# Performance work log

Measured on AMD Instinct MI355X. Metric: run time of the kernel, lower is better.

Reference implementation:

```python
import jax, jax.numpy as jnp
import numpy as np

T, B, F = 160, 640, 40
HID, PROJ, LAYERS = 768, 256, 3


def lstm_proj_layer(x, Wk, b, Wp, reverse=False):
    # x: [T, B, in]; Wk: [in+PROJ, 4*HID]; b: [4*HID]; Wp: [HID, PROJ]
    nb = x.shape[1]
    c0 = jnp.zeros((nb, HID), x.dtype)
    h0 = jnp.zeros((nb, PROJ), x.dtype)

    def step(carry, xt):
        c, h = carry
        z = jnp.concatenate([xt, h], axis=-1) @ Wk + b
        i, j, f, o = jnp.split(z, 4, axis=-1)  # TF LSTMCell gate order i,j,f,o
        c = jax.nn.sigmoid(f + 1.0) * c + jax.nn.sigmoid(i) * jnp.tanh(j)  # forget_bias=1.0
        h = (jax.nn.sigmoid(o) * jnp.tanh(c)) @ Wp  # projection
        return (c, h), h

    _, ys = jax.lax.scan(step, (c0, h0), x, reverse=reverse)
    return ys  # [T, B, PROJ], time-aligned with input even when reverse=True


def _run_stack(x, params, reverse):
    for (Wk, b, Wp) in params:
        x = lstm_proj_layer(x, Wk, b, Wp, reverse=reverse)
    return x


def setup_inputs() -> dict:
    key = jax.random.key(0)
    keys = jax.random.split(key, 1 + 6 * LAYERS)
    inp = {"batch": jax.random.normal(keys[0], (T, B, F), dtype=jnp.float32)}
    ki = 1
    for d in ("fw", "bw"):
        for l in range(LAYERS):
            in_dim = F if l == 0 else PROJ
            inp[f"Wk_{d}{l}"] = jax.random.normal(keys[ki], (in_dim + PROJ, 4 * HID), dtype=jnp.float32) * 0.05
            inp[f"b_{d}{l}"] = jnp.zeros((4 * HID,), dtype=jnp.float32)
            inp[f"Wp_{d}{l}"] = jax.random.normal(keys[ki + 1], (HID, PROJ), dtype=jnp.float32) * 0.05
            ki += 2
    return inp


def reference(batch,
              Wk_fw0, b_fw0, Wp_fw0, Wk_fw1, b_fw1, Wp_fw1, Wk_fw2, b_fw2, Wp_fw2,
              Wk_bw0, b_bw0, Wp_bw0, Wk_bw1, b_bw1, Wp_bw1, Wk_bw2, b_bw2, Wp_bw2):
    fw_params = [(Wk_fw0, b_fw0, Wp_fw0), (Wk_fw1, b_fw1, Wp_fw1), (Wk_fw2, b_fw2, Wp_fw2)]
    bw_params = [(Wk_bw0, b_bw0, Wp_bw0), (Wk_bw1, b_bw1, Wp_bw1), (Wk_bw2, b_bw2, Wp_bw2)]
    out_fw = _run_stack(batch, fw_params, reverse=False)
    out_bw = _run_stack(batch, bw_params, reverse=True)
    outputs = jnp.concatenate([out_fw, out_bw], axis=2)  # [T, B, 2*PROJ]
    embedded = (outputs[0] + outputs[-1]) / 2.0
    # tf.nn.l2_normalize semantics
    embedded = embedded * jax.lax.rsqrt(jnp.maximum(jnp.sum(embedded * embedded, axis=-1, keepdims=True), 1e-12))
    return embedded
```

## Files before the change

kernel.cpp:

```cpp
#include <hip/hip_runtime.h>


typedef _Float16 h8 __attribute__((ext_vector_type(8)));
typedef float f4 __attribute__((ext_vector_type(4)));

#define T_STEPS 160
#define NB 640
#define HID 768
#define PROJ 256
#define NGATE 3072

__device__ __forceinline__ float sigm(float x) { return 1.0f / (1.0f + __expf(-x)); }
__device__ __forceinline__ float tanh_fast(float x) { return 2.0f / (1.0f + __expf(-2.0f * x)) - 1.0f; }

struct GateArgs {
  const _Float16* A0[6];
  const _Float16* A1[6];
  const _Float16* Bw[6];
  const float*    bias[6];
  float*          cst[6];
  _Float16*       g[6];
  int w0[6];
  int lda0[6];
  int K[6];
  int act[6];
};

struct ProjArgs {
  const _Float16* G[6];
  const _Float16* Wp[6];
  _Float16* out[6];
  _Float16* out2[6];
  int act[6];
};

__global__ __launch_bounds__(512) void gate_step(GateArgs args) {
  const int z = blockIdx.z;
  if (!args.act[z]) return;

  __shared__ __align__(16) char sm[33280];
  _Float16 (*As)[72] = (_Float16(*)[72])sm;
  _Float16 (*Bs)[72] = (_Float16(*)[72])(sm + 18432);
  float (*zs)[65] = (float(*)[65])sm;

  const _Float16* A0 = args.A0[z];
  const _Float16* A1 = args.A1[z];
  const _Float16* Bw = args.Bw[z];
  const int w0 = args.w0[z], lda0 = args.lda0[z], K = args.K[z];
  const int n0 = blockIdx.x * 64;
  const int m0 = blockIdx.y * 128;
  const int tid = threadIdx.x;
  const int lane = tid & 63;
  const int wv = tid >> 6;
  const int wm = (wv & 3) * 32;
  const int wn = (wv >> 2) * 32;

  f4 acc[2][2] = {};

  const int lr = tid >> 3;
  const int lkg = (tid & 7) * 8;

  for (int k0 = 0; k0 < K; k0 += 64) {
    const int gk = k0 + lkg;
    h8 av0, av1;
    if (gk < w0) {
      av0 = *(const h8*)(A0 + (size_t)(m0 + lr) * lda0 + gk);
      av1 = *(const h8*)(A0 + (size_t)(m0 + lr + 64) * lda0 + gk);
    } else {
      av0 = *(const h8*)(A1 + (size_t)(m0 + lr) * 256 + (gk - w0));
      av1 = *(const h8*)(A1 + (size_t)(m0 + lr + 64) * 256 + (gk - w0));
    }
    h8 bv = *(const h8*)(Bw + (size_t)(n0 + lr) * K + gk);
    __syncthreads();
    *(h8*)&As[lr][lkg] = av0;
    *(h8*)&As[lr + 64][lkg] = av1;
    *(h8*)&Bs[lr][lkg] = bv;
    __syncthreads();
    const int mr = wm + (lane & 15);
    const int nr = wn + (lane & 15);
#pragma unroll
    for (int kk = 0; kk < 2; ++kk) {
      const int kq = ((lane >> 4) * 8) + kk * 32;
      h8 a0 = *(const h8*)&As[mr][kq];
      h8 a1 = *(const h8*)&As[mr + 16][kq];
      h8 b0 = *(const h8*)&Bs[nr][kq];
      h8 b1 = *(const h8*)&Bs[nr + 16][kq];
      acc[0][0] = __builtin_amdgcn_mfma_f32_16x16x32_f16(a0, b0, acc[0][0], 0, 0, 0);
      acc[0][1] = __builtin_amdgcn_mfma_f32_16x16x32_f16(a0, b1, acc[0][1], 0, 0, 0);
      acc[1][0] = __builtin_amdgcn_mfma_f32_16x16x32_f16(a1, b0, acc[1][0], 0, 0, 0);
      acc[1][1] = __builtin_amdgcn_mfma_f32_16x16x32_f16(a1, b1, acc[1][1], 0, 0, 0);
    }
  }

  __syncthreads();
#pragma unroll
  for (int mi = 0; mi < 2; ++mi)
#pragma unroll
    for (int ni = 0; ni < 2; ++ni)
#pragma unroll
      for (int r = 0; r < 4; ++r) {
        int row = wm + mi * 16 + ((lane >> 4) << 2) + r;
        int col = wn + ni * 16 + (lane & 15);
        zs[row][col] = acc[mi][ni][r];
      }
  __syncthreads();

  const float* bias = args.bias[z];
  float* cstate = args.cst[z];
  _Float16* gout = args.g[z];
  const int u0 = n0 >> 2;
#pragma unroll
  for (int it = 0; it < 4; ++it) {
    int item = it * 512 + tid;
    int row = item >> 4;
    int u = item & 15;
    float zi = zs[row][4 * u + 0] + bias[0 * HID + u0 + u];
    float zj = zs[row][4 * u + 1] + bias[1 * HID + u0 + u];
    float zf = zs[row][4 * u + 2] + bias[2 * HID + u0 + u];
    float zo = zs[row][4 * u + 3] + bias[3 * HID + u0 + u];
    size_t co = (size_t)(m0 + row) * HID + u0 + u;
    float cold = cstate[co];
    float cnew = sigm(zf + 1.0f) * cold + sigm(zi) * tanh_fast(zj);
    float g = sigm(zo) * tanh_fast(cnew);
    cstate[co] = cnew;
    gout[co] = (_Float16)g;
  }
}

__global__ __launch_bounds__(256) void proj_step(ProjArgs args) {
  const int z = blockIdx.z;
  if (!args.act[z]) return;

  __shared__ __align__(16) _Float16 As[64][72];
  __shared__ __align__(16) _Float16 Bs[64][72];

  const _Float16* A = args.G[z];
  const _Float16* B = args.Wp[z];
  const int n0 = blockIdx.x * 64;
  const int m0 = blockIdx.y * 64;
  const int tid = threadIdx.x;
  const int lane = tid & 63;
  const int wv = tid >> 6;
  const int wm = (wv & 1) * 32;
  const int wn = (wv >> 1) * 32;

  f4 acc[2][2] = {};
  const int lr = tid >> 3;
  const int lkg = (tid & 7) * 8;

  for (int k0 = 0; k0 < HID; k0 += 64) {
    const int gk = k0 + lkg;
    h8 av0 = *(const h8*)(A + (size_t)(m0 + lr) * HID + gk);
    h8 av1 = *(const h8*)(A + (size_t)(m0 + lr + 32) * HID + gk);
    h8 bv0 = *(const h8*)(B + (size_t)(n0 + lr) * HID + gk);
    h8 bv1 = *(const h8*)(B + (size_t)(n0 + lr + 32) * HID + gk);
    __syncthreads();
    *(h8*)&As[lr][lkg] = av0;
    *(h8*)&As[lr + 32][lkg] = av1;
    *(h8*)&Bs[lr][lkg] = bv0;
    *(h8*)&Bs[lr + 32][lkg] = bv1;
    __syncthreads();
    const int mr = wm + (lane & 15);
    const int nr = wn + (lane & 15);
#pragma unroll
    for (int kk = 0; kk < 2; ++kk) {
      const int kq = ((lane >> 4) * 8) + kk * 32;
      h8 a0 = *(const h8*)&As[mr][kq];
      h8 a1 = *(const h8*)&As[mr + 16][kq];
      h8 b0 = *(const h8*)&Bs[nr][kq];
      h8 b1 = *(const h8*)&Bs[nr + 16][kq];
      acc[0][0] = __builtin_amdgcn_mfma_f32_16x16x32_f16(a0, b0, acc[0][0], 0, 0, 0);
      acc[0][1] = __builtin_amdgcn_mfma_f32_16x16x32_f16(a0, b1, acc[0][1], 0, 0, 0);
      acc[1][0] = __builtin_amdgcn_mfma_f32_16x16x32_f16(a1, b0, acc[1][0], 0, 0, 0);
      acc[1][1] = __builtin_amdgcn_mfma_f32_16x16x32_f16(a1, b1, acc[1][1], 0, 0, 0);
    }
  }

  _Float16* outp = args.out[z];
  _Float16* out2 = args.out2[z];
#pragma unroll
  for (int mi = 0; mi < 2; ++mi)
#pragma unroll
    for (int ni = 0; ni < 2; ++ni)
#pragma unroll
      for (int r = 0; r < 4; ++r) {
        int row = wm + mi * 16 + ((lane >> 4) << 2) + r;
        int col = wn + ni * 16 + (lane & 15);
        _Float16 v = (_Float16)acc[mi][ni][r];
        size_t o = (size_t)(m0 + row) * PROJ + (n0 + col);
        outp[o] = v;
        if (out2) out2[o] = v;
      }
}

__global__ void convX(const float* __restrict__ X, _Float16* __restrict__ X16, size_t total) {
  size_t i = (size_t)blockIdx.x * 256 + threadIdx.x;
  if (i >= total) return;
  int p = (int)(i & 63);
  size_t tb = i >> 6;
  float v = (p < 40) ? X[tb * 40 + p] : 0.0f;
  X16[i] = (_Float16)v;
}

__global__ void conv_wk(const float* __restrict__ Wk, _Float16* __restrict__ out,
                        int mode, int Kpad, size_t total) {
  size_t i = (size_t)blockIdx.x * 256 + threadIdx.x;
  if (i >= total) return;
  int k = (int)(i % Kpad);
  int n = (int)(i / Kpad);
  int u = n >> 2, g = n & 3;
  int col = g * HID + u;
  float v;
  if (mode == 0) {
    if (k < 40)      v = Wk[(size_t)k * NGATE + col];
    else if (k < 64) v = 0.0f;
    else             v = Wk[(size_t)(k - 24) * NGATE + col];
  } else {
    v = Wk[(size_t)k * NGATE + col];
  }
  out[i] = (_Float16)v;
}

__global__ void conv_wp(const float* __restrict__ Wp, _Float16* __restrict__ out, size_t total) {
  size_t i = (size_t)blockIdx.x * 256 + threadIdx.x;
  if (i >= total) return;
  int k = (int)(i % HID);
  int c = (int)(i / HID);
  out[i] = (_Float16)Wp[(size_t)k * PROJ + c];
}

__global__ __launch_bounds__(256) void readout(const _Float16* __restrict__ E, float* __restrict__ out) {
  const size_t SL = (size_t)NB * PROJ;
  int b = blockIdx.x, tid = threadIdx.x;
  float v[2];
  float ss = 0.0f;
#pragma unroll
  for (int i = 0; i < 2; ++i) {
    int j = tid + i * 256;
    int d = j >> 8, c = j & 255;
    const _Float16* base = E + (size_t)d * 2 * SL;
    float a = (float)base[(size_t)b * PROJ + c];
    float z = (float)base[SL + (size_t)b * PROJ + c];
    v[i] = 0.5f * (a + z);
    ss += v[i] * v[i];
  }
#pragma unroll
  for (int off = 32; off; off >>= 1) ss += __shfl_down(ss, off);
  __shared__ float ps[4];
  if ((tid & 63) == 0) ps[tid >> 6] = ss;
  __syncthreads();
  float tot = ps[0] + ps[1] + ps[2] + ps[3];
  float nrm = rsqrtf(fmaxf(tot, 1e-12f));
  out[(size_t)b * 512 + tid] = v[0] * nrm;
  out[(size_t)b * 512 + tid + 256] = v[1] * nrm;
}

extern "C" void kernel_launch(void* const* d_in, const int* in_sizes, int n_in,
                              void* d_out, int out_size, void* d_ws, size_t ws_size,
                              hipStream_t stream) {
  (void)in_sizes; (void)n_in; (void)out_size; (void)ws_size;
  const float* X = (const float*)d_in[0];
  const float* Wk[2][3]; const float* Bi[2][3]; const float* Wp[2][3];
  for (int d = 0; d < 2; ++d)
    for (int l = 0; l < 3; ++l) {
      int base = 1 + d * 9 + l * 3;
      Wk[d][l] = (const float*)d_in[base];
      Bi[d][l] = (const float*)d_in[base + 1];
      Wp[d][l] = (const float*)d_in[base + 2];
    }

  char* ws = (char*)d_ws;
  size_t off = 0;
  auto alloc = [&](size_t bytes) -> void* {
    void* p = ws + off;
    off += (bytes + 255) & ~(size_t)255;
    return p;
  };

  const size_t SL = (size_t)NB * PROJ;

  _Float16* X16 = (_Float16*)alloc((size_t)T_STEPS * NB * 64 * 2);
  _Float16* WkT[2][3];
  for (int d = 0; d < 2; ++d)
    for (int l = 0; l < 3; ++l)
      WkT[d][l] = (_Float16*)alloc((size_t)NGATE * (l == 0 ? 320 : 512) * 2);
  _Float16* WpT[2][3];
  for (int d = 0; d < 2; ++d)
    for (int l = 0; l < 3; ++l)
      WpT[d][l] = (_Float16*)alloc((size_t)PROJ * HID * 2);
  _Float16* Hbuf = (_Float16*)alloc(6UL * 4 * SL * 2);
  float* cst = (float*)alloc(6UL * NB * HID * 4);
  _Float16* gbuf = (_Float16*)alloc(6UL * NB * HID * 2);
  _Float16* embed = (_Float16*)alloc(4UL * SL * 2);

  auto Hslot = [&](int l, int d, int slot) -> _Float16* {
    return Hbuf + (((size_t)(l * 2 + d) * 4) + slot) * SL;
  };

  {
    size_t tot = (size_t)T_STEPS * NB * 64;
    convX<<<dim3((unsigned)((tot + 255) / 256)), 256, 0, stream>>>(X, X16, tot);
  }
  for (int d = 0; d < 2; ++d)
    for (int l = 0; l < 3; ++l) {
      int Kpad = (l == 0) ? 320 : 512;
      size_t tot = (size_t)NGATE * Kpad;
      conv_wk<<<dim3((unsigned)((tot + 255) / 256)), 256, 0, stream>>>(
          Wk[d][l], WkT[d][l], (l == 0) ? 0 : 1, Kpad, tot);
      size_t totp = (size_t)PROJ * HID;
      conv_wp<<<dim3((unsigned)((totp + 255) / 256)), 256, 0, stream>>>(Wp[d][l], WpT[d][l], totp);
    }
  hipMemsetAsync(Hbuf, 0, 6UL * 4 * SL * 2, stream);
  hipMemsetAsync(cst, 0, 6UL * NB * HID * 4, stream);

  for (int s = 0; s <= 161; ++s) {
    GateArgs ga{};
    ProjArgs pa{};
    for (int l = 0; l < 3; ++l)
      for (int d = 0; d < 2; ++d) {
        int z = l * 2 + d;
        int t = s - l;
        if (t < 0 || t > 159) { ga.act[z] = 0; pa.act[z] = 0; continue; }
        int tt = (d == 0) ? t : 159 - t;
        ga.act[z] = 1; pa.act[z] = 1;
        if (l == 0) {
          ga.A0[z] = X16 + (size_t)tt * NB * 64;
          ga.w0[z] = 64; ga.lda0[z] = 64; ga.K[z] = 320;
        } else {
          ga.A0[z] = Hslot(l - 1, d, (tt + 1) & 3);
          ga.w0[z] = 256; ga.lda0[z] = 256; ga.K[z] = 512;
        }
        int rdslot = (d == 0) ? (tt & 3) : ((tt + 2) & 3);
        ga.A1[z] = Hslot(l, d, rdslot);
        ga.Bw[z] = WkT[d][l];
        ga.bias[z] = Bi[d][l];
        ga.cst[z] = cst + (size_t)z * NB * HID;
        ga.g[z] = gbuf + (size_t)z * NB * HID;

        pa.G[z] = gbuf + (size_t)z * NB * HID;
        pa.Wp[z] = WpT[d][l];
        pa.out[z] = Hslot(l, d, (tt + 1) & 3);
        pa.out2[z] = nullptr;
        if (l == 2 && (tt == 0 || tt == 159))
          pa.out2[z] = embed + ((size_t)d * 2 + (tt == 0 ? 0 : 1)) * SL;
      }
    gate_step<<<dim3(48, 5, 6), 512, 0, stream>>>(ga);
    proj_step<<<dim3(4, 10, 6), 256, 0, stream>>>(pa);
  }

  readout<<<dim3(NB), 256, 0, stream>>>(embed, (float*)d_out);
}
```

Measured before the change: 6.124 ms.

## Enlarge gate GEMM tile to 128x128 and load tiles via global_load_lds DMA

The gate-step GEMM now gives each block a 128x128 output tile with 4 waves, each computing a 64x64 tile of 4x4 MFMA fragments. Tiles are copied straight from global memory into LDS with global_load_lds, stored in fragment-native order so each lane reads its operands without padding or register staging. The aim is higher arithmetic intensity per LDS read and less load-instruction overhead. In exchange the grid has half as many blocks (720 instead of 1440), which reduces parallelism, and the epilogue must stage the accumulators through LDS in two passes.

```diff
diff --git a/kernel.cpp b/kernel.cpp
--- a/kernel.cpp
+++ b/kernel.cpp
@@ -12,6 +12,12 @@
 
 __device__ __forceinline__ float sigm(float x) { return 1.0f / (1.0f + __expf(-x)); }
 __device__ __forceinline__ float tanh_fast(float x) { return 2.0f / (1.0f + __expf(-2.0f * x)) - 1.0f; }
+
+typedef __attribute__((address_space(1))) const void gas_t;
+typedef __attribute__((address_space(3))) void las_t;
+__device__ __forceinline__ void dma16(void* lds, const void* g) {
+  __builtin_amdgcn_global_load_lds((gas_t*)g, (las_t*)lds, 16, 0, 0);
+}
 
 struct GateArgs {
   const _Float16* A0[6];
@@ -34,96 +40,101 @@
   int act[6];
 };
 
-__global__ __launch_bounds__(512) void gate_step(GateArgs args) {
+__global__ __launch_bounds__(256) void gate_step(GateArgs args) {
   const int z = blockIdx.z;
   if (!args.act[z]) return;
 
   __shared__ __align__(16) char sm[33280];
-  _Float16 (*As)[72] = (_Float16(*)[72])sm;
-  _Float16 (*Bs)[72] = (_Float16(*)[72])(sm + 18432);
+  char* smA = sm;
+  char* smB = sm + 16384;
   float (*zs)[65] = (float(*)[65])sm;
 
   const _Float16* A0 = args.A0[z];
   const _Float16* A1 = args.A1[z];
   const _Float16* Bw = args.Bw[z];
   const int w0 = args.w0[z], lda0 = args.lda0[z], K = args.K[z];
-  const int n0 = blockIdx.x * 64;
+  const int n0 = blockIdx.x * 128;
   const int m0 = blockIdx.y * 128;
   const int tid = threadIdx.x;
   const int lane = tid & 63;
   const int wv = tid >> 6;
-  const int wm = (wv & 3) * 32;
-  const int wn = (wv >> 2) * 32;
-
-  f4 acc[2][2] = {};
-
-  const int lr = tid >> 3;
-  const int lkg = (tid & 7) * 8;
+  const int wm = (wv & 1) * 64;
+  const int wn = (wv >> 1) * 64;
+
+  f4 acc[4][4] = {};
+
+  const int mrow = lane & 15;
+  const int kcol = (lane >> 4) * 8;
 
   for (int k0 = 0; k0 < K; k0 += 64) {
-    const int gk = k0 + lkg;
-    h8 av0, av1;
-    if (gk < w0) {
-      av0 = *(const h8*)(A0 + (size_t)(m0 + lr) * lda0 + gk);
-      av1 = *(const h8*)(A0 + (size_t)(m0 + lr + 64) * lda0 + gk);
-    } else {
-      av0 = *(const h8*)(A1 + (size_t)(m0 + lr) * 256 + (gk - w0));
-      av1 = *(const h8*)(A1 + (size_t)(m0 + lr + 64) * 256 + (gk - w0));
-    }
-    h8 bv = *(const h8*)(Bw + (size_t)(n0 + lr) * K + gk);
-    __syncthreads();
-    *(h8*)&As[lr][lkg] = av0;
-    *(h8*)&As[lr + 64][lkg] = av1;
-    *(h8*)&Bs[lr][lkg] = bv;
-    __syncthreads();
-    const int mr = wm + (lane & 15);
-    const int nr = wn + (lane & 15);
+    __syncthreads();
+    const _Float16* Asrc; int Alda, kof;
+    if (k0 < w0) { Asrc = A0; Alda = lda0; kof = k0; }
+    else         { Asrc = A1; Alda = 256;  kof = k0 - w0; }
+#pragma unroll
+    for (int j = 0; j < 4; ++j) {
+      int q = wv + 4 * j;
+      int mi = q >> 1, kk = q & 1;
+      dma16(smA + q * 1024,
+            Asrc + (size_t)(m0 + mi * 16 + mrow) * Alda + kof + kk * 32 + kcol);
+      dma16(smB + q * 1024,
+            Bw + (size_t)(n0 + mi * 16 + mrow) * K + k0 + kk * 32 + kcol);
+    }
+    __syncthreads();
 #pragma unroll
     for (int kk = 0; kk < 2; ++kk) {
-      const int kq = ((lane >> 4) * 8) + kk * 32;
-      h8 a0 = *(const h8*)&As[mr][kq];
-      h8 a1 = *(const h8*)&As[mr + 16][kq];
-      h8 b0 = *(const h8*)&Bs[nr][kq];
-      h8 b1 = *(const h8*)&Bs[nr + 16][kq];
-      acc[0][0] = __builtin_amdgcn_mfma_f32_16x16x32_f16(a0, b0, acc[0][0], 0, 0, 0);
-      acc[0][1] = __builtin_amdgcn_mfma_f32_16x16x32_f16(a0, b1, acc[0][1], 0, 0, 0);
-      acc[1][0] = __builtin_amdgcn_mfma_f32_16x16x32_f16(a1, b0, acc[1][0], 0, 0, 0);
-      acc[1][1] = __builtin_amdgcn_mfma_f32_16x16x32_f16(a1, b1, acc[1][1], 0, 0, 0);
-    }
-  }
-
-  __syncthreads();
-#pragma unroll
-  for (int mi = 0; mi < 2; ++mi)
-#pragma unroll
-    for (int ni = 0; ni < 2; ++ni)
-#pragma unroll
-      for (int r = 0; r < 4; ++r) {
-        int row = wm + mi * 16 + ((lane >> 4) << 2) + r;
-        int col = wn + ni * 16 + (lane & 15);
-        zs[row][col] = acc[mi][ni][r];
+      h8 af[4], bf[4];
+#pragma unroll
+      for (int i = 0; i < 4; ++i) {
+        int miA = (wm >> 4) + i;
+        int niB = (wn >> 4) + i;
+        af[i] = *(const h8*)(smA + (miA * 2 + kk) * 1024 + lane * 16);
+        bf[i] = *(const h8*)(smB + (niB * 2 + kk) * 1024 + lane * 16);
       }
-  __syncthreads();
+#pragma unroll
+      for (int i = 0; i < 4; ++i)
+#pragma unroll
+        for (int jn = 0; jn < 4; ++jn)
+          acc[i][jn] = __builtin_amdgcn_mfma_f32_16x16x32_f16(af[i], bf[jn], acc[i][jn], 0, 0, 0);
+    }
+  }
 
   const float* bias = args.bias[z];
   float* cstate = args.cst[z];
   _Float16* gout = args.g[z];
-  const int u0 = n0 >> 2;
-#pragma unroll
-  for (int it = 0; it < 4; ++it) {
-    int item = it * 512 + tid;
-    int row = item >> 4;
-    int u = item & 15;
-    float zi = zs[row][4 * u + 0] + bias[0 * HID + u0 + u];
-    float zj = zs[row][4 * u + 1] + bias[1 * HID + u0 + u];
-    float zf = zs[row][4 * u + 2] + bias[2 * HID + u0 + u];
-    float zo = zs[row][4 * u + 3] + bias[3 * HID + u0 + u];
-    size_t co = (size_t)(m0 + row) * HID + u0 + u;
-    float cold = cstate[co];
-    float cnew = sigm(zf + 1.0f) * cold + sigm(zi) * tanh_fast(zj);
-    float g = sigm(zo) * tanh_fast(cnew);
-    cstate[co] = cnew;
-    gout[co] = (_Float16)g;
+#pragma unroll
+  for (int p = 0; p < 2; ++p) {
+    __syncthreads();
+    if ((wv >> 1) == p) {
+#pragma unroll
+      for (int mi = 0; mi < 4; ++mi)
+#pragma unroll
+        for (int ni = 0; ni < 4; ++ni)
+#pragma unroll
+          for (int r = 0; r < 4; ++r) {
+            int row = wm + mi * 16 + ((lane >> 4) << 2) + r;
+            int col = ni * 16 + (lane & 15);
+            zs[row][col] = acc[mi][ni][r];
+          }
+    }
+    __syncthreads();
+    const int u0 = (n0 + p * 64) >> 2;
+#pragma unroll
+    for (int it = 0; it < 8; ++it) {
+      int item = it * 256 + tid;
+      int row = item >> 4;
+      int u = item & 15;
+      float zi = zs[row][4 * u + 0] + bias[0 * HID + u0 + u];
+      float zj = zs[row][4 * u + 1] + bias[1 * HID + u0 + u];
+      float zf = zs[row][4 * u + 2] + bias[2 * HID + u0 + u];
+      float zo = zs[row][4 * u + 3] + bias[3 * HID + u0 + u];
+      size_t co = (size_t)(m0 + row) * HID + u0 + u;
+      float cold = cstate[co];
+      float cnew = sigm(zf + 1.0f) * cold + sigm(zi) * tanh_fast(zj);
+      float g = sigm(zo) * tanh_fast(cnew);
+      cstate[co] = cnew;
+      gout[co] = (_Float16)g;
+    }
   }
 }
 
@@ -240,8 +251,8 @@
     int d = j >> 8, c = j & 255;
     const _Float16* base = E + (size_t)d * 2 * SL;
     float a = (float)base[(size_t)b * PROJ + c];
-    float z = (float)base[SL + (size_t)b * PROJ + c];
-    v[i] = 0.5f * (a + z);
+    float zv = (float)base[SL + (size_t)b * PROJ + c];
+    v[i] = 0.5f * (a + zv);
     ss += v[i] * v[i];
   }
 #pragma unroll
@@ -344,7 +355,7 @@
         if (l == 2 && (tt == 0 || tt == 159))
           pa.out2[z] = embed + ((size_t)d * 2 + (tt == 0 ? 0 : 1)) * SL;
       }
-    gate_step<<<dim3(48, 5, 6), 512, 0, stream>>>(ga);
+    gate_step<<<dim3(24, 5, 6), 256, 0, stream>>>(ga);
     proj_step<<<dim3(4, 10, 6), 256, 0, stream>>>(pa);
   }
 
```

Measured after the change: 8.304 ms. +35.6%, slower.
